# Optimization experiments

Hardware: AMD Instinct MI355X
Metric: run time of the kernel (lower is better)

The kernel has to match this reference:

```python
import jax, jax.numpy as jnp
import numpy as np


def setup_inputs() -> dict:
    B, n, emb, K = 8, 128, 256, 8
    N = B * n            # total nodes
    Eg = n               # edges per graph (one out-edge per node)
    E = B * Eg           # total edges
    E2 = E * K           # total edge-to-edge edges
    key = jax.random.key(0)
    k1, k2, k3, k4 = jax.random.split(key, 4)
    x = jax.random.normal(k1, (N, emb), jnp.float32)
    edge_attr = jax.random.normal(k2, (E, emb), jnp.float32)
    enc_W = jax.random.normal(k3, (3, emb), jnp.float32)
    e2e_W = jax.random.normal(k4, (3, emb), jnp.float32)
    # deterministic simple-graph edges: node i -> node (i+1) mod n within each graph
    e = np.arange(E); g = e // Eg; el = e % Eg
    src = g * n + el
    dst = g * n + (el + 1) % n
    edge_index = jnp.asarray(np.stack([src, dst]), jnp.int32)
    batch_vec = jnp.asarray(np.arange(N) // n, jnp.int32)
    # e2e graph: edge-node s connected to edge-nodes (s+1..s+K) mod Eg within graph
    f = np.arange(E2); fg = f // (Eg * K); fl = f % (Eg * K)
    s_e = fl % Eg; d_e = (s_e + 1 + fl // Eg) % Eg
    e2e_edge_index = jnp.asarray(np.stack([fg * Eg + s_e, fg * Eg + d_e]), jnp.int32)
    e_batch = jnp.asarray(np.arange(E) // Eg, jnp.int32)
    # each e2e edge carries features of the dst node of its source edge
    e2e_node_index = jnp.asarray(dst[fg * Eg + s_e], jnp.int32)
    return {"x": x, "edge_attr": edge_attr, "enc_W": enc_W, "e2e_W": e2e_W,
            "edge_index": edge_index, "batch_vec": batch_vec,
            "e2e_edge_index": e2e_edge_index, "e_batch": e_batch,
            "e2e_node_index": e2e_node_index, "n_graphs": B}


def _offsets(bvec, B):
    # start offset of each graph in the packed (node or edge) dimension
    counts = jax.ops.segment_sum(jnp.ones_like(bvec), bvec, num_segments=B)
    return jnp.concatenate([jnp.zeros((1,), counts.dtype), jnp.cumsum(counts)[:-1]])


def reference(x, edge_attr, enc_W, e2e_W, edge_index, batch_vec,
              e2e_edge_index, e_batch, e2e_node_index, n_graphs):
    B = int(n_graphs)
    N, emb = x.shape
    n = N // B
    E = edge_attr.shape[0]
    Eg = E // B
    mask = jnp.array([0.0, 1.0, 1.0], x.dtype)[:, None]  # Embedding padding_idx=0

    # ---- node-level dense edge features ----
    node_off = _offsets(batch_vec, B)
    src, dst = edge_index[0], edge_index[1]
    g = batch_vec[src]
    li = src - node_off[g]
    lj = dst - node_off[g]
    ea = edge_attr + x[src] + x[dst]                       # [E, emb]
    edge_dense = jnp.zeros((B, n, n, emb), x.dtype).at[g, li, lj].add(ea)
    # edge type codes: 0 = connected, 1 = diagonal, 2 = disconnected
    adj = jnp.zeros((B, n, n), jnp.int32).at[g, li, lj].add(2)
    lall = jnp.arange(N) - node_off[batch_vec]
    adj = adj.at[batch_vec, lall, lall].add(1)
    edge_dense = edge_dense + (enc_W * mask)[2 - adj]

    # ---- edge-to-edge dense features ----
    x2 = x + jax.ops.segment_sum(edge_attr, dst, num_segments=N)
    e_off = _offsets(e_batch, B)
    es, ed = e2e_edge_index[0], e2e_edge_index[1]
    eg = e_batch[es]
    eli = es - e_off[eg]
    elj = ed - e_off[eg]
    e2e_dense = jnp.zeros((B, Eg, Eg, emb), x.dtype).at[eg, eli, elj].add(x2[e2e_node_index])
    adj2 = jnp.zeros((B, Eg, Eg), jnp.int32).at[eg, eli, elj].add(2)
    leall = jnp.arange(E) - e_off[e_batch]
    adj2 = adj2.at[e_batch, leall, leall].add(1)
    e2e_dense = e2e_dense + (e2e_W * mask)[2 - adj2]

    return edge_dense, e2e_dense
```

## Files before the change

### kernel.cpp

```cpp
#include <hip/hip_runtime.h>

#define MAXB 1024

__global__ void offsets_k(const int* __restrict__ bv, int N,
                          const int* __restrict__ eb, int E,
                          const int* __restrict__ nG,
                          int* __restrict__ node_off, int* __restrict__ e_off) {
    __shared__ int c1[MAXB];
    __shared__ int c2[MAXB];
    int B = nG[0];
    if (B > MAXB) B = MAXB;
    for (int i = threadIdx.x; i < B; i += blockDim.x) { c1[i] = 0; c2[i] = 0; }
    __syncthreads();
    for (int i = threadIdx.x; i < N; i += blockDim.x) atomicAdd(&c1[bv[i]], 1);
    for (int i = threadIdx.x; i < E; i += blockDim.x) atomicAdd(&c2[eb[i]], 1);
    __syncthreads();
    if (threadIdx.x == 0) {
        int a = 0, b = 0;
        for (int g = 0; g < B; ++g) {
            node_off[g] = a; a += c1[g];
            e_off[g]    = b; b += c2[g];
        }
    }
}

__global__ void x2_copy_k(const float4* __restrict__ x, float4* __restrict__ x2, int n4) {
    int t = blockIdx.x * blockDim.x + threadIdx.x;
    if (t < n4) x2[t] = x[t];
}

__global__ void x2_add_k(const float* __restrict__ edge_attr,
                         const int* __restrict__ edge_index,
                         int E, int emb, float* __restrict__ x2) {
    int t = blockIdx.x * blockDim.x + threadIdx.x;
    if (t >= E * emb) return;
    int e = t / emb;
    int c = t - e * emb;
    int dst = edge_index[E + e];
    atomicAdd(&x2[dst * emb + c], edge_attr[t]);
}

__global__ void fill_k(float4* __restrict__ out, unsigned int total4,
                       const float4* __restrict__ encW,
                       const float4* __restrict__ e2eW,
                       const int* __restrict__ nG,
                       int N, int E, int emb4) {
    int B = nG[0];
    unsigned int n  = (unsigned int)(N / B);
    unsigned int Eg = (unsigned int)(E / B);
    unsigned int uemb4 = (unsigned int)emb4;
    unsigned int edge4 = (unsigned int)N * n * uemb4;
    unsigned int stride = gridDim.x * blockDim.x;
    for (unsigned int idx = blockIdx.x * blockDim.x + threadIdx.x; idx < total4; idx += stride) {
        unsigned int r = idx;
        const float4* W = encW;
        unsigned int dim = n;
        if (r >= edge4) { r -= edge4; W = e2eW; dim = Eg; }
        unsigned int cell = r / uemb4;
        unsigned int c4 = r - cell * uemb4;
        unsigned int j = cell % dim;
        unsigned int i = (cell / dim) % dim;
        out[idx] = (i == j) ? W[uemb4 + c4] : W[2u * uemb4 + c4];
    }
}

__global__ void scatter_edge_k(const float4* __restrict__ edge_attr,
                               const float4* __restrict__ x,
                               const int* __restrict__ edge_index,
                               const int* __restrict__ bv,
                               const int* __restrict__ node_off,
                               const float4* __restrict__ encW,
                               const int* __restrict__ nG,
                               int N, int E, int emb4,
                               float4* __restrict__ out) {
    int t = blockIdx.x * blockDim.x + threadIdx.x;
    if (t >= E * emb4) return;
    int e = t / emb4;
    int c4 = t - e * emb4;
    int src = edge_index[e];
    int dst = edge_index[E + e];
    int g = bv[src];
    int B = nG[0];
    int n = N / B;
    int li = src - node_off[g];
    int lj = dst - node_off[g];
    float4 a  = edge_attr[t];
    float4 xs = x[(long)src * emb4 + c4];
    float4 xd = x[(long)dst * emb4 + c4];
    float4 v;
    v.x = a.x + xs.x + xd.x;
    v.y = a.y + xs.y + xd.y;
    v.z = a.z + xs.z + xd.z;
    v.w = a.w + xs.w + xd.w;
    if (li == lj) {
        float4 wv = encW[2 * emb4 + c4];
        v.x += wv.x; v.y += wv.y; v.z += wv.z; v.w += wv.w;
    }
    long addr = ((long)(g * n + li) * n + lj) * emb4 + c4;
    out[addr] = v;
}

__global__ void scatter_e2e_k(const float* __restrict__ x2f,
                              const int* __restrict__ e2e_ei,
                              const int* __restrict__ eb,
                              const int* __restrict__ e_off,
                              const int* __restrict__ e2e_nidx,
                              const float4* __restrict__ e2eW,
                              const int* __restrict__ nG,
                              int N, int E, int E2, int emb4,
                              float4* __restrict__ out) {
    int t = blockIdx.x * blockDim.x + threadIdx.x;
    if (t >= E2 * emb4) return;
    int f = t / emb4;
    int c4 = t - f * emb4;
    int es = e2e_ei[f];
    int ed = e2e_ei[E2 + f];
    int g = eb[es];
    int B = nG[0];
    int n = N / B;
    int Eg = E / B;
    int eli = es - e_off[g];
    int elj = ed - e_off[g];
    const float4* x2 = (const float4*)x2f;
    float4 v = x2[(long)e2e_nidx[f] * emb4 + c4];
    if (eli == elj) {
        float4 wv = e2eW[2 * emb4 + c4];
        v.x += wv.x; v.y += wv.y; v.z += wv.z; v.w += wv.w;
    }
    long edge4 = (long)N * n * emb4;
    long addr = edge4 + ((long)(g * Eg + eli) * Eg + elj) * emb4 + c4;
    out[addr] = v;
}

extern "C" void kernel_launch(void* const* d_in, const int* in_sizes, int n_in,
                              void* d_out, int out_size, void* d_ws, size_t ws_size,
                              hipStream_t stream) {
    const float* x          = (const float*)d_in[0];
    const float* edge_attr  = (const float*)d_in[1];
    const float* enc_W      = (const float*)d_in[2];
    const float* e2e_W      = (const float*)d_in[3];
    const int* edge_index   = (const int*)d_in[4];
    const int* batch_vec    = (const int*)d_in[5];
    const int* e2e_ei       = (const int*)d_in[6];
    const int* e_batch      = (const int*)d_in[7];
    const int* e2e_nidx     = (const int*)d_in[8];
    const int* nG           = (const int*)d_in[9];

    int emb  = in_sizes[2] / 3;
    int emb4 = emb / 4;
    int N    = in_sizes[0] / emb;
    int E    = in_sizes[1] / emb;
    int E2   = in_sizes[8];

    char* ws      = (char*)d_ws;
    int* node_off = (int*)ws;
    int* e_off    = (int*)(ws + 4096);
    float* x2     = (float*)(ws + 8192);

    offsets_k<<<1, 256, 0, stream>>>(batch_vec, N, e_batch, E, nG, node_off, e_off);

    int n4x = (N * emb) / 4;
    x2_copy_k<<<(n4x + 255) / 256, 256, 0, stream>>>((const float4*)x, (float4*)x2, n4x);

    int tadd = E * emb;
    x2_add_k<<<(tadd + 255) / 256, 256, 0, stream>>>(edge_attr, edge_index, E, emb, x2);

    unsigned int total4 = (unsigned int)(out_size / 4);
    fill_k<<<8192, 256, 0, stream>>>((float4*)d_out, total4,
                                     (const float4*)enc_W, (const float4*)e2e_W,
                                     nG, N, E, emb4);

    int t1 = E * emb4;
    scatter_edge_k<<<(t1 + 255) / 256, 256, 0, stream>>>(
        (const float4*)edge_attr, (const float4*)x, edge_index, batch_vec,
        node_off, (const float4*)enc_W, nG, N, E, emb4, (float4*)d_out);

    int t2 = E2 * emb4;
    scatter_e2e_k<<<(t2 + 255) / 256, 256, 0, stream>>>(
        x2, e2e_ei, e_batch, e_off, e2e_nidx,
        (const float4*)e2e_W, nG, N, E, E2, emb4, (float4*)d_out);
}
```

Baseline: 292.7 us.

## Replace fill-then-scatter with cell map and single write-once output kernel

Builds an integer map per dense output cell recording the source edge or node index plus a diagonal flag, then one kernel writes each output row exactly once from that map. This removes the double writes of the fill pass followed by scatter passes, and the per-element div/mod index math. It adds extra launches, a map buffer in the workspace, and a map read per cell.

Result: no change. 292.8 us (+0.1%).

```diff
diff --git a/kernel.cpp b/kernel.cpp
--- a/kernel.cpp
+++ b/kernel.cpp
@@ -1,6 +1,7 @@
 #include <hip/hip_runtime.h>
 
 #define MAXB 1024
+#define DIAGF 0x40000000
 
 __global__ void offsets_k(const int* __restrict__ bv, int N,
                           const int* __restrict__ eb, int E,
@@ -24,6 +25,60 @@
     }
 }
 
+__global__ void map_init_k(int* __restrict__ map, int C) {
+    int stride = gridDim.x * blockDim.x;
+    for (int i = blockIdx.x * blockDim.x + threadIdx.x; i < C; i += stride)
+        map[i] = -1;
+}
+
+__global__ void map_diag_k(const int* __restrict__ nG, int N, int E,
+                           int* __restrict__ map) {
+    int t = blockIdx.x * blockDim.x + threadIdx.x;
+    if (t >= N + E) return;
+    int B = nG[0];
+    int n = N / B, Eg = E / B;
+    int C1 = N * n;
+    int cell;
+    if (t < N) {
+        int g = t / n, l = t - g * n;
+        cell = (g * n + l) * n + l;
+    } else {
+        int u = t - N;
+        int g = u / Eg, l = u - g * Eg;
+        cell = C1 + (g * Eg + l) * Eg + l;
+    }
+    map[cell] = -2;
+}
+
+__global__ void map_scatter_k(const int* __restrict__ ei,
+                              const int* __restrict__ bv,
+                              const int* __restrict__ node_off,
+                              const int* __restrict__ e2e_ei,
+                              const int* __restrict__ eb,
+                              const int* __restrict__ e_off,
+                              const int* __restrict__ nidx,
+                              const int* __restrict__ nG,
+                              int N, int E, int E2, int* __restrict__ map) {
+    int t = blockIdx.x * blockDim.x + threadIdx.x;
+    if (t >= E + E2) return;
+    int B = nG[0];
+    int n = N / B, Eg = E / B;
+    int C1 = N * n;
+    if (t < E) {
+        int e = t;
+        int s = ei[e], d = ei[E + e];
+        int g = bv[s];
+        int li = s - node_off[g], lj = d - node_off[g];
+        map[(g * n + li) * n + lj] = e | (li == lj ? DIAGF : 0);
+    } else {
+        int f = t - E;
+        int es = e2e_ei[f], ed = e2e_ei[E2 + f];
+        int g = eb[es];
+        int li = es - e_off[g], lj = ed - e_off[g];
+        map[C1 + (g * Eg + li) * Eg + lj] = nidx[f] | (li == lj ? DIAGF : 0);
+    }
+}
+
 __global__ void x2_copy_k(const float4* __restrict__ x, float4* __restrict__ x2, int n4) {
     int t = blockIdx.x * blockDim.x + threadIdx.x;
     if (t < n4) x2[t] = x[t];
@@ -40,96 +95,54 @@
     atomicAdd(&x2[dst * emb + c], edge_attr[t]);
 }
 
-__global__ void fill_k(float4* __restrict__ out, unsigned int total4,
-                       const float4* __restrict__ encW,
-                       const float4* __restrict__ e2eW,
-                       const int* __restrict__ nG,
-                       int N, int E, int emb4) {
-    int B = nG[0];
-    unsigned int n  = (unsigned int)(N / B);
-    unsigned int Eg = (unsigned int)(E / B);
-    unsigned int uemb4 = (unsigned int)emb4;
-    unsigned int edge4 = (unsigned int)N * n * uemb4;
-    unsigned int stride = gridDim.x * blockDim.x;
-    for (unsigned int idx = blockIdx.x * blockDim.x + threadIdx.x; idx < total4; idx += stride) {
-        unsigned int r = idx;
-        const float4* W = encW;
-        unsigned int dim = n;
-        if (r >= edge4) { r -= edge4; W = e2eW; dim = Eg; }
-        unsigned int cell = r / uemb4;
-        unsigned int c4 = r - cell * uemb4;
-        unsigned int j = cell % dim;
-        unsigned int i = (cell / dim) % dim;
-        out[idx] = (i == j) ? W[uemb4 + c4] : W[2u * uemb4 + c4];
-    }
-}
-
-__global__ void scatter_edge_k(const float4* __restrict__ edge_attr,
-                               const float4* __restrict__ x,
-                               const int* __restrict__ edge_index,
-                               const int* __restrict__ bv,
-                               const int* __restrict__ node_off,
-                               const float4* __restrict__ encW,
-                               const int* __restrict__ nG,
-                               int N, int E, int emb4,
-                               float4* __restrict__ out) {
-    int t = blockIdx.x * blockDim.x + threadIdx.x;
-    if (t >= E * emb4) return;
-    int e = t / emb4;
-    int c4 = t - e * emb4;
-    int src = edge_index[e];
-    int dst = edge_index[E + e];
-    int g = bv[src];
+__global__ __launch_bounds__(256) void main_k(
+    const int* __restrict__ map,
+    const float4* __restrict__ edge_attr,
+    const float4* __restrict__ x,
+    const float4* __restrict__ x2,
+    const int* __restrict__ ei,
+    const float4* __restrict__ encW,
+    const float4* __restrict__ e2eW,
+    const int* __restrict__ nG,
+    int N, int E, int emb4, int C,
+    float4* __restrict__ out) {
     int B = nG[0];
     int n = N / B;
-    int li = src - node_off[g];
-    int lj = dst - node_off[g];
-    float4 a  = edge_attr[t];
-    float4 xs = x[(long)src * emb4 + c4];
-    float4 xd = x[(long)dst * emb4 + c4];
-    float4 v;
-    v.x = a.x + xs.x + xd.x;
-    v.y = a.y + xs.y + xd.y;
-    v.z = a.z + xs.z + xd.z;
-    v.w = a.w + xs.w + xd.w;
-    if (li == lj) {
-        float4 wv = encW[2 * emb4 + c4];
-        v.x += wv.x; v.y += wv.y; v.z += wv.z; v.w += wv.w;
+    int C1 = N * n;
+    int lane = threadIdx.x & 63;
+    int wave = (blockIdx.x * blockDim.x + threadIdx.x) >> 6;
+    int nw   = (gridDim.x * blockDim.x) >> 6;
+    for (int cell = wave; cell < C; cell += nw) {
+        int m = map[cell];
+        const float4* W = (cell < C1) ? encW : e2eW;
+        for (int c4 = lane; c4 < emb4; c4 += 64) {
+            float4 v;
+            if (m == -1) {
+                v = W[2 * emb4 + c4];
+            } else if (m == -2) {
+                v = W[emb4 + c4];
+            } else {
+                int id = m & 0x3FFFFFFF;
+                if (cell < C1) {
+                    int s = ei[id], d = ei[E + id];
+                    float4 a  = edge_attr[(long)id * emb4 + c4];
+                    float4 xs = x[(long)s * emb4 + c4];
+                    float4 xd = x[(long)d * emb4 + c4];
+                    v.x = a.x + xs.x + xd.x;
+                    v.y = a.y + xs.y + xd.y;
+                    v.z = a.z + xs.z + xd.z;
+                    v.w = a.w + xs.w + xd.w;
+                } else {
+                    v = x2[(long)id * emb4 + c4];
+                }
+                if (m & DIAGF) {
+                    float4 w2 = W[2 * emb4 + c4];
+                    v.x += w2.x; v.y += w2.y; v.z += w2.z; v.w += w2.w;
+                }
+            }
+            out[(long)cell * emb4 + c4] = v;
+        }
     }
-    long addr = ((long)(g * n + li) * n + lj) * emb4 + c4;
-    out[addr] = v;
-}
-
-__global__ void scatter_e2e_k(const float* __restrict__ x2f,
-                              const int* __restrict__ e2e_ei,
-                              const int* __restrict__ eb,
-                              const int* __restrict__ e_off,
-                              const int* __restrict__ e2e_nidx,
-                              const float4* __restrict__ e2eW,
-                              const int* __restrict__ nG,
-                              int N, int E, int E2, int emb4,
-                              float4* __restrict__ out) {
-    int t = blockIdx.x * blockDim.x + threadIdx.x;
-    if (t >= E2 * emb4) return;
-    int f = t / emb4;
-    int c4 = t - f * emb4;
-    int es = e2e_ei[f];
-    int ed = e2e_ei[E2 + f];
-    int g = eb[es];
-    int B = nG[0];
-    int n = N / B;
-    int Eg = E / B;
-    int eli = es - e_off[g];
-    int elj = ed - e_off[g];
-    const float4* x2 = (const float4*)x2f;
-    float4 v = x2[(long)e2e_nidx[f] * emb4 + c4];
-    if (eli == elj) {
-        float4 wv = e2eW[2 * emb4 + c4];
-        v.x += wv.x; v.y += wv.y; v.z += wv.z; v.w += wv.w;
-    }
-    long edge4 = (long)N * n * emb4;
-    long addr = edge4 + ((long)(g * Eg + eli) * Eg + elj) * emb4 + c4;
-    out[addr] = v;
 }
 
 extern "C" void kernel_launch(void* const* d_in, const int* in_sizes, int n_in,
@@ -151,13 +164,23 @@
     int N    = in_sizes[0] / emb;
     int E    = in_sizes[1] / emb;
     int E2   = in_sizes[8];
+    int C    = out_size / emb;
 
     char* ws      = (char*)d_ws;
     int* node_off = (int*)ws;
     int* e_off    = (int*)(ws + 4096);
     float* x2     = (float*)(ws + 8192);
+    int* map      = (int*)(ws + 8192 + (size_t)N * emb * 4);
 
     offsets_k<<<1, 256, 0, stream>>>(batch_vec, N, e_batch, E, nG, node_off, e_off);
+
+    map_init_k<<<1024, 256, 0, stream>>>(map, C);
+
+    map_diag_k<<<(N + E + 255) / 256, 256, 0, stream>>>(nG, N, E, map);
+
+    map_scatter_k<<<(E + E2 + 255) / 256, 256, 0, stream>>>(
+        edge_index, batch_vec, node_off, e2e_ei, e_batch, e_off,
+        e2e_nidx, nG, N, E, E2, map);
 
     int n4x = (N * emb) / 4;
     x2_copy_k<<<(n4x + 255) / 256, 256, 0, stream>>>((const float4*)x, (float4*)x2, n4x);
@@ -165,18 +188,8 @@
     int tadd = E * emb;
     x2_add_k<<<(tadd + 255) / 256, 256, 0, stream>>>(edge_attr, edge_index, E, emb, x2);
 
-    unsigned int total4 = (unsigned int)(out_size / 4);
-    fill_k<<<8192, 256, 0, stream>>>((float4*)d_out, total4,
-                                     (const float4*)enc_W, (const float4*)e2e_W,
-                                     nG, N, E, emb4);
-
-    int t1 = E * emb4;
-    scatter_edge_k<<<(t1 + 255) / 256, 256, 0, stream>>>(
-        (const float4*)edge_attr, (const float4*)x, edge_index, batch_vec,
-        node_off, (const float4*)enc_W, nG, N, E, emb4, (float4*)d_out);
-
-    int t2 = E2 * emb4;
-    scatter_e2e_k<<<(t2 + 255) / 256, 256, 0, stream>>>(
-        x2, e2e_ei, e_batch, e_off, e2e_nidx,
-        (const float4*)e2e_W, nG, N, E, E2, emb4, (float4*)d_out);
+    main_k<<<8192, 256, 0, stream>>>(
+        map, (const float4*)edge_attr, (const float4*)x, (const float4*)x2,
+        edge_index, (const float4*)enc_W, (const float4*)e2e_W,
+        nG, N, E, emb4, C, (float4*)d_out);
 }
```
